# Kernel optimization log

Measured on AMD Instinct MI355X. Metric: run time of the kernel, lower is better.

## Reference

```python
import jax, jax.numpy as jnp
import numpy as np

V_PATCH_NUMS = (1, 2, 4, 6, 8, 10, 13, 16)
HW = 16
QUANT_RESI = 0.5
SHARE_K = 4
BETA = 1.0


def _pool_matrix(n_in, n_out):
    # adaptive average pooling as a [n_out, n_in] matrix (matches F.adaptive_avg_pool2d bins)
    P = np.zeros((n_out, n_in), np.float32)
    for i in range(n_out):
        s = (i * n_in) // n_out
        e = -((-(i + 1) * n_in) // n_out)  # ceil((i+1)*n_in/n_out)
        P[i, s:e] = 1.0 / (e - s)
    return jnp.asarray(P)


def _phi_index(si, SN):
    # PhiPartiallyShared.__getitem__(si/(SN-1)) with K=4 ticks
    K = SHARE_K
    ticks = np.linspace(1.0 / 3 / K, 1 - 1.0 / 3 / K, K) if K == 4 else np.linspace(1.0 / 2 / K, 1 - 1.0 / 2 / K, K)
    return int(np.argmin(np.abs(ticks - si / (SN - 1))))


def _phi(h, w, b):
    # Phi: h*(1-r) + conv3x3(h)*r, zero padding (nn.Conv2d default)
    y = jax.lax.conv_general_dilated(h, w, (1, 1), 'SAME',
                                     dimension_numbers=('NCHW', 'OIHW', 'NCHW'))
    y = y + b[None, :, None, None]
    return h * (1.0 - QUANT_RESI) + y * QUANT_RESI


def setup_inputs() -> dict:
    key = jax.random.key(0)
    k0, k1, k2 = jax.random.split(key, 3)
    B, C, V = 64, 32, 4096
    f = jax.random.normal(k0, (B, C, HW, HW), jnp.float32)
    embed = jax.random.normal(k1, (V, C), jnp.float32)  # EMAEmbedding.weight ~ randn
    phi_w = jax.random.normal(k2, (SHARE_K, C, C, 3, 3), jnp.float32) * (1.0 / np.sqrt(9.0 * C))
    phi_b = jnp.zeros((SHARE_K, C), jnp.float32)
    return {"f_BChw": f, "embed_weight": embed, "phi_w": phi_w, "phi_b": phi_b}


def reference(f_BChw, embed_weight, phi_w, phi_b):
    B, C, H, W = f_BChw.shape
    SN = len(V_PATCH_NUMS)
    f_ng = jax.lax.stop_gradient(f_BChw)
    f_hat = jnp.zeros_like(f_BChw)
    e_sq = jnp.sum(embed_weight * embed_weight, axis=1)  # [V]
    loss = jnp.float32(0.0)
    for si, pn in enumerate(V_PATCH_NUMS):
        rest = f_ng - jax.lax.stop_gradient(f_hat)  # residual to quantize (no grad through distance)
        if pn != H:
            P = _pool_matrix(H, pn)
            rest_d = jnp.einsum('oh,bchw,pw->bcop', P, rest, P)  # adaptive avg pool -> [B,C,pn,pn]
        else:
            rest_d = rest
        rest_NC = rest_d.transpose(0, 2, 3, 1).reshape(-1, C)  # [B*pn*pn, C]
        # squared euclidean cdist to codebook, argmin
        d = (jnp.sum(rest_NC * rest_NC, axis=1, keepdims=True)
             + e_sq[None, :]
             - 2.0 * (rest_NC @ embed_weight.T))  # [N, V]
        idx = jnp.argmin(d, axis=1)  # [B*pn*pn] int
        h = embed_weight[idx].reshape(B, pn, pn, C).transpose(0, 3, 1, 2)  # gather -> [B,C,pn,pn]
        if pn != H:
            h = jax.image.resize(h, (B, C, H, W), method='linear')  # bilinear, align_corners=False
        k = _phi_index(si, SN)
        h = _phi(h, phi_w[k], phi_b[k])
        f_hat = f_hat + h
        loss = loss + 0.25 * jnp.mean((jax.lax.stop_gradient(f_hat) - f_BChw) ** 2) \
                    + BETA * jnp.mean((f_hat - f_ng) ** 2)
    loss = loss / SN
    # straight-through estimator: grads flow to f_BChw as identity
    f_hat_st = jax.lax.stop_gradient(f_hat - f_BChw) + f_BChw
    return f_hat_st, loss
```

## Files before the change

kernel.cpp:

```cpp
#include <hip/hip_runtime.h>
#include <hip/hip_bf16.h>

#define BB 64
#define CC 32
#define HW2 256
#define VV 4096
#define NELEM (BB*CC*HW2)
#define NPAD 16640

#define OFF_F     0
#define OFF_FHAT  (OFF_F     + NELEM)
#define OFF_EMB   (OFF_FHAT  + NELEM)
#define OFF_ESQ   (OFF_EMB   + VV*CC)
#define OFF_PW    (OFF_ESQ   + VV)
#define OFF_PB    (OFF_PW    + 4*CC*CC*9)
#define OFF_REST  (OFF_PB    + 4*CC)
#define OFF_BESTA (OFF_REST  + CC*NPAD)
#define OFF_BESTB (OFF_BESTA + 2*NPAD)
#define OFF_LOSS  (OFF_BESTB + 2*NPAD)
#define OFF_FLAG  (OFF_LOSS  + 1)

__global__ void k_probe(const void* __restrict__ fin, int* __restrict__ flag) {
    __shared__ int cnt[256];
    int t = threadIdx.x;
    const __hip_bfloat16* p = (const __hip_bfloat16*)fin;
    int local = 0;
    for (int i = t; i < 8192; i += 256) {
        float v = __bfloat162float(p[i]);
        if (!(fabsf(v) < 1e3f)) local++;
    }
    cnt[t] = local;
    __syncthreads();
    for (int s = 128; s > 0; s >>= 1) {
        if (t < s) cnt[t] += cnt[t + s];
        __syncthreads();
    }
    if (t == 0) *flag = (cnt[0] >= 64) ? 1 : 0;
}

__global__ void k_prep(const void* __restrict__ fin,
                       const void* __restrict__ ein,
                       const void* __restrict__ win,
                       const void* __restrict__ bin_,
                       const int* __restrict__ flag,
                       float* __restrict__ f, float* __restrict__ fhat,
                       float* __restrict__ emb, float* __restrict__ pw,
                       float* __restrict__ pb, float* __restrict__ loss) {
    bool isf32 = (*flag != 0);
    int i = blockIdx.x * 256 + threadIdx.x;
    if (i < NELEM) {
        f[i] = isf32 ? ((const float*)fin)[i]
                     : __bfloat162float(((const __hip_bfloat16*)fin)[i]);
        fhat[i] = 0.f;
    }
    if (i < VV*CC)
        emb[i] = isf32 ? ((const float*)ein)[i]
                       : __bfloat162float(((const __hip_bfloat16*)ein)[i]);
    if (i < 4*CC*CC*9)
        pw[i] = isf32 ? ((const float*)win)[i]
                      : __bfloat162float(((const __hip_bfloat16*)win)[i]);
    if (i < 4*CC)
        pb[i] = isf32 ? ((const float*)bin_)[i]
                      : __bfloat162float(((const __hip_bfloat16*)bin_)[i]);
    if (i == 0) *loss = 0.f;
}

__global__ void k_esq(const float* __restrict__ emb, float* __restrict__ esq) {
    int v = blockIdx.x * 256 + threadIdx.x;
    if (v >= VV) return;
    const float* e = emb + v * CC;
    float s = 0.f;
    #pragma unroll
    for (int c = 0; c < CC; ++c) s = fmaf(e[c], e[c], s);
    esq[v] = s;
}

__global__ void k_pool0(const float* __restrict__ f, const float* __restrict__ fhat,
                        float* __restrict__ rest_t, unsigned long long* __restrict__ best) {
    int n = threadIdx.x;
    int c = blockIdx.y;
    if (n >= BB) return;
    if (c == 0) best[n] = 0xFFFFFFFFFFFFFFFFull;
    const float* fb = f + (n * CC + c) * HW2;
    const float* hb = fhat + (n * CC + c) * HW2;
    float s = 0.f;
    for (int h = 0; h < 16; ++h)
        for (int w = 0; w < 16; ++w)
            s += fb[h * 16 + w] - hb[h * 16 + w];
    rest_t[c * NPAD + n] = s * (1.f / 256.f);
}

template<int VPT>
__global__ __launch_bounds__(256, 1)
void k_argmin1(const float* __restrict__ rest_t, const float* __restrict__ emb,
               const float* __restrict__ esq, unsigned long long* __restrict__ best,
               int Ntot, int cpw) {
    int tid = threadIdx.x;
    int base = blockIdx.x * (256 * VPT) + tid;
    int v0 = blockIdx.y * cpw;
    float x[VPT][CC];
    bool valid[VPT];
    int nidx[VPT];
    #pragma unroll
    for (int p = 0; p < VPT; ++p) {
        int n = base + p * 256;
        nidx[p] = n;
        valid[p] = (n < Ntot);
        int nc = valid[p] ? n : 0;
        #pragma unroll
        for (int c = 0; c < CC; ++c) x[p][c] = rest_t[c * NPAD + nc];
    }
    #pragma unroll
    for (int p = 0; p < VPT; ++p)
        #pragma unroll
        for (int c = 0; c < CC; ++c)
            asm volatile("" : "+v"(x[p][c]));
    float xx[VPT];
    #pragma unroll
    for (int p = 0; p < VPT; ++p) {
        float s = 0.f;
        #pragma unroll
        for (int c = 0; c < CC; ++c) s = fmaf(x[p][c], x[p][c], s);
        xx[p] = s;
    }
    float bd[VPT];
    int bi[VPT];
    #pragma unroll
    for (int p = 0; p < VPT; ++p) { bd[p] = 3.4e38f; bi[p] = v0; }

    #pragma unroll 2
    for (int v = v0; v < v0 + cpw; ++v) {
        const float* e = emb + v * CC;
        float d0[VPT], d1[VPT], d2[VPT], d3[VPT];
        #pragma unroll
        for (int p = 0; p < VPT; ++p) { d0[p]=0.f; d1[p]=0.f; d2[p]=0.f; d3[p]=0.f; }
        #pragma unroll
        for (int c = 0; c < CC; c += 4) {
            float e0 = e[c], e1 = e[c+1], e2 = e[c+2], e3 = e[c+3];
            #pragma unroll
            for (int p = 0; p < VPT; ++p) {
                d0[p] = fmaf(x[p][c],   e0, d0[p]);
                d1[p] = fmaf(x[p][c+1], e1, d1[p]);
                d2[p] = fmaf(x[p][c+2], e2, d2[p]);
                d3[p] = fmaf(x[p][c+3], e3, d3[p]);
            }
        }
        float ev = esq[v];
        #pragma unroll
        for (int p = 0; p < VPT; ++p) {
            float dist = (xx[p] + ev) - 2.f * ((d0[p] + d1[p]) + (d2[p] + d3[p]));
            if (dist < bd[p]) { bd[p] = dist; bi[p] = v; }
        }
    }
    #pragma unroll
    for (int p = 0; p < VPT; ++p) {
        if (valid[p]) {
            unsigned u = __float_as_uint(bd[p]);
            unsigned long long mono = (u & 0x80000000u)
                ? (unsigned long long)(~u)
                : (unsigned long long)(u | 0x80000000u);
            atomicMin(best + nidx[p], (mono << 32) | (unsigned long long)(unsigned)bi[p]);
        }
    }
}

__global__ __launch_bounds__(512)
void k_fuse(const float* __restrict__ emb,
            const unsigned long long* __restrict__ best,
            const float* __restrict__ pw, const float* __restrict__ pb,
            const float* __restrict__ f, float* __restrict__ fhat,
            float* __restrict__ loss,
            float* __restrict__ rest_t,
            unsigned long long* __restrict__ best_next,
            int pn, int k, int pn_next) {
    __shared__ float h_up[CC][HW2];
    __shared__ float extra[CC * 169];
    __shared__ float red[8];
    int b = blockIdx.x, coq = blockIdx.y, t = threadIdx.x;
    int nn = pn * pn;
    int pix = t & 255, half = t >> 8;
    int y = pix >> 4, x = pix & 15;
    int c0 = half * 16;

    if (pn == 16) {
        int id = (int)(unsigned)(best[b * HW2 + pix] & 0xFFFFFFFFull);
        const float* er = emb + id * CC + c0;
        #pragma unroll
        for (int c = 0; c < 16; ++c) h_up[c0 + c][pix] = er[c];
    } else {
        float (*hs)[169] = (float(*)[169])extra;
        for (int cell = t; cell < nn; cell += 512) {
            int id = (int)(unsigned)(best[b * nn + cell] & 0xFFFFFFFFull);
            const float* er = emb + id * CC;
            #pragma unroll
            for (int c = 0; c < CC; ++c) hs[c][cell] = er[c];
        }
        __syncthreads();
        float scale = (float)pn / 16.f;
        float sy = (y + 0.5f) * scale - 0.5f;
        sy = fminf(fmaxf(sy, 0.f), (float)(pn - 1));
        int y0 = (int)sy; int y1 = min(y0 + 1, pn - 1); float wy = sy - (float)y0;
        float sx = (x + 0.5f) * scale - 0.5f;
        sx = fminf(fmaxf(sx, 0.f), (float)(pn - 1));
        int x0 = (int)sx; int x1 = min(x0 + 1, pn - 1); float wx = sx - (float)x0;
        float wy0 = 1.f - wy, wx0 = 1.f - wx;
        #pragma unroll
        for (int c = 0; c < 16; ++c) {
            int cc = c0 + c;
            float v00 = hs[cc][y0 * pn + x0], v01 = hs[cc][y0 * pn + x1];
            float v10 = hs[cc][y1 * pn + x0], v11 = hs[cc][y1 * pn + x1];
            float a0 = wy0 * v00 + wy * v10;
            float a1 = wy0 * v01 + wy * v11;
            h_up[cc][pix] = wx0 * a0 + wx * a1;
        }
    }
    __syncthreads();

    float acc[4];
    #pragma unroll
    for (int o = 0; o < 4; ++o) acc[o] = 0.f;
    for (int ci_ = 0; ci_ < CC; ++ci_) {
        float hv[9];
        #pragma unroll
        for (int dy = 0; dy < 3; ++dy)
            #pragma unroll
            for (int dx = 0; dx < 3; ++dx) {
                int yy = y + dy - 1, xx2 = x + dx - 1;
                hv[dy * 3 + dx] = (yy >= 0 && yy < 16 && xx2 >= 0 && xx2 < 16)
                                  ? h_up[ci_][yy * 16 + xx2] : 0.f;
            }
        const float* wp = pw + ((k * CC + coq * 8 + half * 4) * CC + ci_) * 9;
        #pragma unroll
        for (int o = 0; o < 4; ++o) {
            const float* w9 = wp + o * (CC * 9);
            #pragma unroll
            for (int q = 0; q < 9; ++q) acc[o] = fmaf(hv[q], w9[q], acc[o]);
        }
    }

    float* diff = extra;
    float lsum = 0.f;
    #pragma unroll
    for (int o = 0; o < 4; ++o) {
        int lo = half * 4 + o;
        int co = coq * 8 + lo;
        float hval = h_up[co][pix];
        float outv = hval * 0.5f + (acc[o] + pb[k * CC + co]) * 0.5f;
        int pos = (b * CC + co) * HW2 + pix;
        float fh = fhat[pos] + outv;
        fhat[pos] = fh;
        float dd = f[pos] - fh;
        diff[lo * HW2 + pix] = dd;
        lsum = fmaf(dd, dd, lsum);
    }
    #pragma unroll
    for (int off = 32; off > 0; off >>= 1) lsum += __shfl_down(lsum, off, 64);
    if ((t & 63) == 0) red[t >> 6] = lsum;
    __syncthreads();
    if (t == 0) {
        float s = 0.f;
        #pragma unroll
        for (int w = 0; w < 8; ++w) s += red[w];
        atomicAdd(loss, s);
    }

    if (pn_next > 0) {
        int nn2 = pn_next * pn_next;
        for (int q = t; q < nn2 * 8; q += 512) {
            int cell = q % nn2, o = q / nn2;
            int i = cell / pn_next, j = cell % pn_next;
            int s0 = (i * 16) / pn_next, e0 = ((i + 1) * 16 + pn_next - 1) / pn_next;
            int s1 = (j * 16) / pn_next, e1 = ((j + 1) * 16 + pn_next - 1) / pn_next;
            float inv = 1.f / (float)((e0 - s0) * (e1 - s1));
            float s = 0.f;
            for (int h = s0; h < e0; ++h)
                for (int w = s1; w < e1; ++w)
                    s += diff[o * HW2 + h * 16 + w];
            rest_t[(coq * 8 + o) * NPAD + b * nn2 + cell] = s * inv;
        }
        if (coq == 0)
            for (int q = t; q < nn2; q += 512)
                best_next[b * nn2 + q] = 0xFFFFFFFFFFFFFFFFull;
    }
}

__global__ void k_out(const float* __restrict__ fhat, const float* __restrict__ loss,
                      const int* __restrict__ flag, void* __restrict__ out) {
    bool isf32 = (*flag != 0);
    int i = blockIdx.x * 256 + threadIdx.x;
    if (i > NELEM) return;
    float v;
    if (i < NELEM) v = fhat[i];
    else           v = (*loss) * (1.25f / (float)NELEM / 8.f);
    if (isf32) ((float*)out)[i] = v;
    else       ((__hip_bfloat16*)out)[i] = __float2bfloat16(v);
}

extern "C" void kernel_launch(void* const* d_in, const int* in_sizes, int n_in,
                              void* d_out, int out_size, void* d_ws, size_t ws_size,
                              hipStream_t stream) {
    const void* fin  = d_in[0];
    const void* ein  = d_in[1];
    const void* win  = d_in[2];
    const void* bin_ = d_in[3];
    float* ws = (float*)d_ws;
    float* f    = ws + OFF_F;
    float* fhat = ws + OFF_FHAT;
    float* emb  = ws + OFF_EMB;
    float* esq  = ws + OFF_ESQ;
    float* pw   = ws + OFF_PW;
    float* pb   = ws + OFF_PB;
    float* rest_t = ws + OFF_REST;
    unsigned long long* bestA = (unsigned long long*)(ws + OFF_BESTA);
    unsigned long long* bestB = (unsigned long long*)(ws + OFF_BESTB);
    float* loss = ws + OFF_LOSS;
    int*   flag = (int*)(ws + OFF_FLAG);

    static const int PN[8]  = {1, 2, 4, 6, 8, 10, 13, 16};
    static const int KK[8]  = {0, 0, 1, 1, 2, 2, 3, 3};
    static const int SP[8]  = {64, 64, 64, 64, 64, 32, 32, 32};
    static const int VPT[8] = {1, 1, 1, 1, 2, 2, 2, 2};

    k_probe<<<1, 256, 0, stream>>>(fin, flag);
    k_prep<<<(NELEM + 255) / 256, 256, 0, stream>>>(fin, ein, win, bin_, flag, f, fhat, emb, pw, pb, loss);
    k_esq<<<(VV + 255) / 256, 256, 0, stream>>>(emb, esq);
    k_pool0<<<dim3(1, CC), 256, 0, stream>>>(f, fhat, rest_t, bestA);

    for (int si = 0; si < 8; ++si) {
        int pn = PN[si];
        int Ntot = BB * pn * pn;
        int Sp = SP[si];
        int cpw = VV / Sp;
        unsigned long long* bcur = (si & 1) ? bestB : bestA;
        unsigned long long* bnxt = (si & 1) ? bestA : bestB;
        int pn_next = (si < 7) ? PN[si + 1] : 0;
        if (VPT[si] == 2) {
            int gx = (Ntot + 511) / 512;
            k_argmin1<2><<<dim3(gx, Sp), 256, 0, stream>>>(rest_t, emb, esq, bcur, Ntot, cpw);
        } else {
            int gx = (Ntot + 255) / 256;
            k_argmin1<1><<<dim3(gx, Sp), 256, 0, stream>>>(rest_t, emb, esq, bcur, Ntot, cpw);
        }
        k_fuse<<<dim3(BB, 4), 512, 0, stream>>>(emb, bcur, pw, pb, f, fhat, loss,
                                                rest_t, bnxt, pn, KK[si], pn_next);
    }
    k_out<<<(NELEM + 1 + 255) / 256, 256, 0, stream>>>(fhat, loss, flag, d_out);
}
```

Baseline: 516.9 us.

## Restructure codebook argmin to tile 32 codes per pass with reloaded residual chunks

The argmin kernel stops keeping the full 32-channel residual in registers for one or two points. It now handles one point per thread and builds 32 codeword distances at a time, reloading 8-channel residual slices from global memory for each codeword tile. The codebook split count rises for most scales to add more blocks. The goal is fewer live registers and more independent accumulators, at the cost of repeated residual loads and a different FMA order that may change tie-breaking.

```diff
diff --git a/kernel.cpp b/kernel.cpp
--- a/kernel.cpp
+++ b/kernel.cpp
@@ -90,77 +90,57 @@
     rest_t[c * NPAD + n] = s * (1.f / 256.f);
 }
 
-template<int VPT>
 __global__ __launch_bounds__(256, 1)
-void k_argmin1(const float* __restrict__ rest_t, const float* __restrict__ emb,
-               const float* __restrict__ esq, unsigned long long* __restrict__ best,
-               int Ntot, int cpw) {
-    int tid = threadIdx.x;
-    int base = blockIdx.x * (256 * VPT) + tid;
+void k_argmin(const float* __restrict__ rest_t, const float* __restrict__ emb,
+              const float* __restrict__ esq, unsigned long long* __restrict__ best,
+              int Ntot, int cpw) {
+    int n = blockIdx.x * 256 + threadIdx.x;
+    bool valid = (n < Ntot);
+    int nc = valid ? n : 0;
     int v0 = blockIdx.y * cpw;
-    float x[VPT][CC];
-    bool valid[VPT];
-    int nidx[VPT];
-    #pragma unroll
-    for (int p = 0; p < VPT; ++p) {
-        int n = base + p * 256;
-        nidx[p] = n;
-        valid[p] = (n < Ntot);
-        int nc = valid[p] ? n : 0;
-        #pragma unroll
-        for (int c = 0; c < CC; ++c) x[p][c] = rest_t[c * NPAD + nc];
-    }
-    #pragma unroll
-    for (int p = 0; p < VPT; ++p)
-        #pragma unroll
-        for (int c = 0; c < CC; ++c)
-            asm volatile("" : "+v"(x[p][c]));
-    float xx[VPT];
-    #pragma unroll
-    for (int p = 0; p < VPT; ++p) {
-        float s = 0.f;
-        #pragma unroll
-        for (int c = 0; c < CC; ++c) s = fmaf(x[p][c], x[p][c], s);
-        xx[p] = s;
-    }
-    float bd[VPT];
-    int bi[VPT];
-    #pragma unroll
-    for (int p = 0; p < VPT; ++p) { bd[p] = 3.4e38f; bi[p] = v0; }
-
-    #pragma unroll 2
-    for (int v = v0; v < v0 + cpw; ++v) {
-        const float* e = emb + v * CC;
-        float d0[VPT], d1[VPT], d2[VPT], d3[VPT];
-        #pragma unroll
-        for (int p = 0; p < VPT; ++p) { d0[p]=0.f; d1[p]=0.f; d2[p]=0.f; d3[p]=0.f; }
-        #pragma unroll
-        for (int c = 0; c < CC; c += 4) {
-            float e0 = e[c], e1 = e[c+1], e2 = e[c+2], e3 = e[c+3];
-            #pragma unroll
-            for (int p = 0; p < VPT; ++p) {
-                d0[p] = fmaf(x[p][c],   e0, d0[p]);
-                d1[p] = fmaf(x[p][c+1], e1, d1[p]);
-                d2[p] = fmaf(x[p][c+2], e2, d2[p]);
-                d3[p] = fmaf(x[p][c+3], e3, d3[p]);
+
+    float xx = 0.f;
+    #pragma unroll
+    for (int c = 0; c < CC; ++c) {
+        float xv = rest_t[c * NPAD + nc];
+        xx = fmaf(xv, xv, xx);
+    }
+
+    float bd = 3.4e38f;
+    int bi = v0;
+
+    for (int vt = v0; vt < v0 + cpw; vt += 32) {
+        float dacc[32];
+        #pragma unroll
+        for (int vi = 0; vi < 32; ++vi) dacc[vi] = 0.f;
+
+        #pragma unroll
+        for (int ct = 0; ct < CC; ct += 8) {
+            float xc[8];
+            #pragma unroll
+            for (int c = 0; c < 8; ++c) xc[c] = rest_t[(ct + c) * NPAD + nc];
+            #pragma unroll
+            for (int vi = 0; vi < 32; ++vi) {
+                const float* e = emb + (vt + vi) * CC + ct;
+                #pragma unroll
+                for (int c = 0; c < 8; ++c)
+                    dacc[vi] = fmaf(xc[c], e[c], dacc[vi]);
             }
         }
-        float ev = esq[v];
-        #pragma unroll
-        for (int p = 0; p < VPT; ++p) {
-            float dist = (xx[p] + ev) - 2.f * ((d0[p] + d1[p]) + (d2[p] + d3[p]));
-            if (dist < bd[p]) { bd[p] = dist; bi[p] = v; }
-        }
-    }
-    #pragma unroll
-    for (int p = 0; p < VPT; ++p) {
-        if (valid[p]) {
-            unsigned u = __float_as_uint(bd[p]);
-            unsigned long long mono = (u & 0x80000000u)
-                ? (unsigned long long)(~u)
-                : (unsigned long long)(u | 0x80000000u);
-            atomicMin(best + nidx[p], (mono << 32) | (unsigned long long)(unsigned)bi[p]);
-        }
+
+        #pragma unroll
+        for (int vi = 0; vi < 32; ++vi) {
+            float dist = fmaf(-2.f, dacc[vi], xx + esq[vt + vi]);
+            if (dist < bd) { bd = dist; bi = vt + vi; }
+        }
+    }
+
+    if (valid) {
+        unsigned u = __float_as_uint(bd);
+        unsigned long long mono = (u & 0x80000000u)
+            ? (unsigned long long)(~u)
+            : (unsigned long long)(u | 0x80000000u);
+        atomicMin(best + n, (mono << 32) | (unsigned long long)(unsigned)bi);
     }
 }
 
@@ -316,10 +296,9 @@
     float* loss = ws + OFF_LOSS;
     int*   flag = (int*)(ws + OFF_FLAG);
 
-    static const int PN[8]  = {1, 2, 4, 6, 8, 10, 13, 16};
-    static const int KK[8]  = {0, 0, 1, 1, 2, 2, 3, 3};
-    static const int SP[8]  = {64, 64, 64, 64, 64, 32, 32, 32};
-    static const int VPT[8] = {1, 1, 1, 1, 2, 2, 2, 2};
+    static const int PN[8] = {1, 2, 4, 6, 8, 10, 13, 16};
+    static const int KK[8] = {0, 0, 1, 1, 2, 2, 3, 3};
+    static const int SP[8] = {128, 128, 128, 128, 128, 64, 64, 32};
 
     k_probe<<<1, 256, 0, stream>>>(fin, flag);
     k_prep<<<(NELEM + 255) / 256, 256, 0, stream>>>(fin, ein, win, bin_, flag, f, fhat, emb, pw, pb, loss);
@@ -334,13 +313,8 @@
         unsigned long long* bcur = (si & 1) ? bestB : bestA;
         unsigned long long* bnxt = (si & 1) ? bestA : bestB;
         int pn_next = (si < 7) ? PN[si + 1] : 0;
-        if (VPT[si] == 2) {
-            int gx = (Ntot + 511) / 512;
-            k_argmin1<2><<<dim3(gx, Sp), 256, 0, stream>>>(rest_t, emb, esq, bcur, Ntot, cpw);
-        } else {
-            int gx = (Ntot + 255) / 256;
-            k_argmin1<1><<<dim3(gx, Sp), 256, 0, stream>>>(rest_t, emb, esq, bcur, Ntot, cpw);
-        }
+        int gx = (Ntot + 255) / 256;
+        k_argmin<<<dim3(gx, Sp), 256, 0, stream>>>(rest_t, emb, esq, bcur, Ntot, cpw);
         k_fuse<<<dim3(BB, 4), 512, 0, stream>>>(emb, bcur, pw, pb, f, fhat, loss,
                                                 rest_t, bnxt, pn, KK[si], pn_next);
     }
```

New measurement: 549.7 us. 1.06x slower.
